# Kernel optimization log

Measured on AMD Instinct MI355X. Metric: run time of the kernel, lower is better.

The kernel has to match this reference:

```python
import jax, jax.numpy as jnp
import numpy as np

N_NODES = 100000
N_EDGES = 1600000
F_IN = 500
HIDDEN = 64
N_CLASS = 40


def gcn_conv(x, W, b, src, dst, n_nodes):
    """PyG GCNConv: add self-loops, symmetric deg^-1/2 normalization,
    linear transform then scatter-add aggregation at dst."""
    h = x @ W  # [N, out]
    loop = jnp.arange(n_nodes, dtype=src.dtype)
    s = jnp.concatenate([src, loop])  # sources incl. self-loops
    d = jnp.concatenate([dst, loop])
    deg = jax.ops.segment_sum(jnp.ones_like(d, dtype=h.dtype), d, num_segments=n_nodes)
    dinv = jnp.where(deg > 0, jax.lax.rsqrt(deg), 0.0)
    norm = dinv[s] * dinv[d]  # [E+N]
    msg = h[s] * norm[:, None]  # gather + scale, [E+N, out]
    out = jax.ops.segment_sum(msg, d, num_segments=n_nodes)
    return out + b


def setup_inputs() -> dict:
    key = jax.random.key(0)
    k1, k2, k3, k4 = jax.random.split(key, 4)
    x = jax.random.normal(k1, (N_NODES, F_IN), dtype=jnp.float32)
    edge_index = jax.random.randint(k2, (2, N_EDGES), 0, N_NODES, dtype=jnp.int64)
    # Glorot-style init for GCNConv weights
    W1 = jax.random.normal(k3, (F_IN, HIDDEN), dtype=jnp.float32) / np.sqrt(F_IN)
    b1 = jnp.zeros((HIDDEN,), dtype=jnp.float32)
    W2 = jax.random.normal(k4, (HIDDEN, N_CLASS), dtype=jnp.float32) / np.sqrt(HIDDEN)
    b2 = jnp.zeros((N_CLASS,), dtype=jnp.float32)
    return {"x": x, "W1": W1, "b1": b1, "W2": W2, "b2": b2, "edge_index": edge_index}


def reference(x, W1, b1, W2, b2, edge_index):
    src, dst = edge_index[0], edge_index[1]
    n = x.shape[0]
    h = jax.nn.relu(gcn_conv(x, W1, b1, src, dst, n))
    # dropout is identity in eval mode (F.dropout with training=False)
    out = gcn_conv(h, W2, b2, src, dst, n)
    return jax.nn.log_softmax(out, axis=1)
```

## Files before the change

kernel.cpp:

```cpp
#include <hip/hip_runtime.h>
#include <math.h>

#define N_NODES 100000
#define N_EDGES 1600000
#define F_IN    500
#define HIDDEN  64
#define N_CLASS 40
#define KPAD    512

#define NB   2048
#define NPB  49
#define EPB  16384
#define CAP  1536

typedef __attribute__((ext_vector_type(4))) float f32x4;
typedef __attribute__((ext_vector_type(8))) __bf16 bf16x8;

__device__ __forceinline__ unsigned short f2bf(float f) {
    unsigned int u = __float_as_uint(f);
    u = (u + 0x7FFF + ((u >> 16) & 1)) >> 16;
    return (unsigned short)u;
}

__global__ void k_zero_int(int* p, int n) {
    int i = blockIdx.x * blockDim.x + threadIdx.x;
    if (i < n) p[i] = 0;
}

__global__ void k_prep_w1t(const float* __restrict__ w1, unsigned short* __restrict__ w1t) {
    int idx = blockIdx.x * blockDim.x + threadIdx.x;
    if (idx >= HIDDEN * KPAD) return;
    int n = idx >> 9, k = idx & (KPAD - 1);
    float v = (k < F_IN) ? w1[k * HIDDEN + n] : 0.f;
    w1t[idx] = f2bf(v);
}

__launch_bounds__(1024)
__global__ void k_bhist(const int* __restrict__ dst, int* __restrict__ bcnt, int e) {
    __shared__ int h[NB];
    for (int i = threadIdx.x; i < NB; i += 1024) h[i] = 0;
    __syncthreads();
    int base = blockIdx.x * EPB;
#pragma unroll
    for (int j = 0; j < 16; ++j) {
        int i = base + j * 1024 + threadIdx.x;
        if (i < e) atomicAdd(&h[dst[i] / NPB], 1);
    }
    __syncthreads();
    for (int i = threadIdx.x; i < NB; i += 1024)
        if (h[i]) atomicAdd(&bcnt[i], h[i]);
}

__launch_bounds__(1024)
__global__ void k_bscan(const int* __restrict__ bcnt, int* __restrict__ bptr,
                        int* __restrict__ bcur) {
    __shared__ int s[1024];
    int t = threadIdx.x;
    int a = bcnt[2 * t], b = bcnt[2 * t + 1];
    int v = a + b;
    s[t] = v;
    __syncthreads();
    for (int off = 1; off < 1024; off <<= 1) {
        int u = (t >= off) ? s[t - off] : 0;
        __syncthreads();
        s[t] += u;
        __syncthreads();
    }
    int excl = s[t] - v;
    bptr[2 * t] = excl;     bptr[2 * t + 1] = excl + a;
    bcur[2 * t] = excl;     bcur[2 * t + 1] = excl + a;
    if (t == 1023) bptr[NB] = s[1023];
}

__launch_bounds__(1024)
__global__ void k_bfill(const int* __restrict__ src, const int* __restrict__ dst,
                        int* __restrict__ bcur, int2* __restrict__ ebuf, int e) {
    __shared__ int hist[NB];
    __shared__ int base_[NB];
    for (int i = threadIdx.x; i < NB; i += 1024) hist[i] = 0;
    __syncthreads();
    int b0 = blockIdx.x * EPB;
    int s_[16], d_[16];
#pragma unroll
    for (int j = 0; j < 16; ++j) {
        int i = b0 + j * 1024 + threadIdx.x;
        if (i < e) {
            s_[j] = src[i];
            d_[j] = dst[i];
            atomicAdd(&hist[d_[j] / NPB], 1);
        } else d_[j] = -1;
    }
    __syncthreads();
    for (int i = threadIdx.x; i < NB; i += 1024) {
        int hc = hist[i];
        base_[i] = hc ? atomicAdd(&bcur[i], hc) : 0;
        hist[i] = 0;
    }
    __syncthreads();
#pragma unroll
    for (int j = 0; j < 16; ++j) {
        if (d_[j] >= 0) {
            int bu = d_[j] / NPB;
            int r = atomicAdd(&hist[bu], 1);
            ebuf[base_[bu] + r] = make_int2(s_[j], d_[j]);
        }
    }
}

__launch_bounds__(256)
__global__ void k_bucket_csr(const int2* __restrict__ ebuf, const int* __restrict__ bptr,
                             int* __restrict__ rp, int* __restrict__ col,
                             float* __restrict__ dinv, int n) {
    int b  = blockIdx.x;
    int lo = b * NPB;
    if (lo >= n) return;
    int hi  = min(lo + NPB, n);
    int eb0 = bptr[b], ec = bptr[b + 1] - eb0;

    __shared__ int2 pairs[CAP];
    __shared__ int  hist[NPB];
    __shared__ int  excl[NPB + 1];
    for (int j = threadIdx.x; j < NPB; j += 256) hist[j] = 0;
    __syncthreads();
    for (int i = threadIdx.x; i < ec; i += 256) {
        int2 p = ebuf[eb0 + i];
        if (i < CAP) pairs[i] = p;
        atomicAdd(&hist[p.y - lo], 1);
    }
    __syncthreads();
    if (threadIdx.x == 0) {
        int acc = 0;
        for (int j = 0; j < NPB; ++j) { excl[j] = acc; acc += hist[j]; }
        excl[NPB] = acc;
    }
    __syncthreads();
    for (int j = threadIdx.x; j < hi - lo; j += 256) {
        rp[lo + j]   = eb0 + excl[j];
        dinv[lo + j] = rsqrtf((float)(hist[j] + 1));
    }
    if (hi == n && threadIdx.x == 0) rp[n] = eb0 + ec;
    __syncthreads();
    for (int j = threadIdx.x; j < NPB; j += 256) hist[j] = 0;
    __syncthreads();
    for (int i = threadIdx.x; i < ec; i += 256) {
        int2 p  = (i < CAP) ? pairs[i] : ebuf[eb0 + i];
        int  li = p.y - lo;
        int  r  = atomicAdd(&hist[li], 1);
        col[eb0 + excl[li] + r] = p.x;
    }
}

__launch_bounds__(256)
__global__ void k_gemm1(const float* __restrict__ x, const unsigned short* __restrict__ w1t,
                        float* __restrict__ h, int n) {
    __shared__ unsigned short xs[4][32][40];
    const int tid  = threadIdx.x;
    const int wave = tid >> 6;
    const int lane = tid & 63;
    const int quad = lane >> 4;
    const int l16  = lane & 15;
    const int rowb = blockIdx.x * 128 + wave * 32;

    const int srow = lane >> 3;
    const int skof = (lane & 7) * 4;

    f32x4 acc[2][4];
#pragma unroll
    for (int rt = 0; rt < 2; ++rt)
#pragma unroll
        for (int ct = 0; ct < 4; ++ct) acc[rt][ct] = (f32x4)0.f;

    for (int ks = 0; ks < 16; ++ks) {
        const int k0 = ks * 32;

        float4 tmp[4];
        if (ks < 15) {
#pragma unroll
            for (int u = 0; u < 4; ++u) {
                int grow = rowb + u * 8 + srow;
                tmp[u] = (grow < n) ? *(const float4*)&x[(size_t)grow * F_IN + k0 + skof]
                                    : make_float4(0.f, 0.f, 0.f, 0.f);
            }
        } else {
#pragma unroll
            for (int u = 0; u < 4; ++u) {
                int grow = rowb + u * 8 + srow;
                const float* p = &x[(size_t)grow * F_IN];
                float v0 = (grow < n && k0 + skof + 0 < F_IN) ? p[k0 + skof + 0] : 0.f;
                float v1 = (grow < n && k0 + skof + 1 < F_IN) ? p[k0 + skof + 1] : 0.f;
                float v2 = (grow < n && k0 + skof + 2 < F_IN) ? p[k0 + skof + 2] : 0.f;
                float v3 = (grow < n && k0 + skof + 3 < F_IN) ? p[k0 + skof + 3] : 0.f;
                tmp[u] = make_float4(v0, v1, v2, v3);
            }
        }
        bf16x8 bfrag[4];
#pragma unroll
        for (int ct = 0; ct < 4; ++ct)
            bfrag[ct] = *(const bf16x8*)&w1t[(ct * 16 + l16) * KPAD + k0 + quad * 8];

#pragma unroll
        for (int u = 0; u < 4; ++u) {
            unsigned int lo = (unsigned int)f2bf(tmp[u].x) | ((unsigned int)f2bf(tmp[u].y) << 16);
            unsigned int hi = (unsigned int)f2bf(tmp[u].z) | ((unsigned int)f2bf(tmp[u].w) << 16);
            *(uint2*)&xs[wave][u * 8 + srow][skof] = make_uint2(lo, hi);
        }
        __syncthreads();

        union { bf16x8 v; unsigned int u[4]; } af[2];
#pragma unroll
        for (int rt = 0; rt < 2; ++rt) {
            uint2 a = *(const uint2*)&xs[wave][rt * 16 + l16][quad * 8];
            uint2 b = *(const uint2*)&xs[wave][rt * 16 + l16][quad * 8 + 4];
            af[rt].u[0] = a.x; af[rt].u[1] = a.y; af[rt].u[2] = b.x; af[rt].u[3] = b.y;
        }
#pragma unroll
        for (int rt = 0; rt < 2; ++rt)
#pragma unroll
            for (int ct = 0; ct < 4; ++ct)
                acc[rt][ct] = __builtin_amdgcn_mfma_f32_16x16x32_bf16(
                    af[rt].v, bfrag[ct], acc[rt][ct], 0, 0, 0);
        __syncthreads();
    }

#pragma unroll
    for (int rt = 0; rt < 2; ++rt) {
#pragma unroll
        for (int reg = 0; reg < 4; ++reg) {
            int grow = rowb + rt * 16 + quad * 4 + reg;
            if (grow < n) {
#pragma unroll
                for (int ct = 0; ct < 4; ++ct)
                    h[(size_t)grow * HIDDEN + ct * 16 + l16] = acc[rt][ct][reg];
            }
        }
    }
}

template <int F, bool RELU, bool LSM>
__global__ void k_agg(const float* __restrict__ h, const int* __restrict__ rp,
                      const int* __restrict__ col, const float* __restrict__ dinv,
                      const float* __restrict__ bias, float* __restrict__ out, int n) {
    int wid  = (blockIdx.x * blockDim.x + threadIdx.x) >> 6;
    int lane = threadIdx.x & 63;
    if (wid >= n) return;
    int beg = rp[wid], end = rp[wid + 1];
    float acc = 0.f;
    int e = beg;
    for (; e + 4 <= end; e += 4) {
        int s0 = col[e], s1 = col[e + 1], s2 = col[e + 2], s3 = col[e + 3];
        float w0 = dinv[s0], w1 = dinv[s1], w2 = dinv[s2], w3 = dinv[s3];
        float h0 = (lane < F) ? h[(size_t)s0 * F + lane] : 0.f;
        float h1 = (lane < F) ? h[(size_t)s1 * F + lane] : 0.f;
        float h2 = (lane < F) ? h[(size_t)s2 * F + lane] : 0.f;
        float h3 = (lane < F) ? h[(size_t)s3 * F + lane] : 0.f;
        acc += w0 * h0 + w1 * h1 + w2 * h2 + w3 * h3;
    }
    for (; e < end; ++e) {
        int s0 = col[e];
        float w0 = dinv[s0];
        float h0 = (lane < F) ? h[(size_t)s0 * F + lane] : 0.f;
        acc += w0 * h0;
    }
    float di    = dinv[wid];
    float selfv = (lane < F) ? h[(size_t)wid * F + lane] : 0.f;
    float r = di * acc + di * di * selfv + ((lane < F) ? bias[lane] : 0.f);
    if (RELU) r = fmaxf(r, 0.f);
    if (LSM) {
        float v = (lane < F) ? r : -INFINITY;
        float m = v;
        for (int off = 32; off; off >>= 1) m = fmaxf(m, __shfl_xor(m, off));
        float ex = (lane < F) ? __expf(v - m) : 0.f;
        float s = ex;
        for (int off = 32; off; off >>= 1) s += __shfl_xor(s, off);
        if (lane < F) out[(size_t)wid * F + lane] = v - m - __logf(s);
    } else {
        if (lane < F) out[(size_t)wid * F + lane] = r;
    }
}

__launch_bounds__(256)
__global__ void k_gemm2(const float* __restrict__ a, const float* __restrict__ w,
                        float* __restrict__ out, int n) {
    __shared__ float ws[HIDDEN * N_CLASS];
    for (int idx = threadIdx.x; idx < HIDDEN * N_CLASS; idx += 256) ws[idx] = w[idx];
    __syncthreads();
    int idx = blockIdx.x * 256 + threadIdx.x;
    if (idx >= n * N_CLASS) return;
    int i = idx / N_CLASS, j = idx - i * N_CLASS;
    float s = 0.f;
#pragma unroll
    for (int k = 0; k < HIDDEN; k += 4) {
        float4 xv = *(const float4*)&a[(size_t)i * HIDDEN + k];
        s = fmaf(xv.x, ws[k * N_CLASS + j], s);
        s = fmaf(xv.y, ws[(k + 1) * N_CLASS + j], s);
        s = fmaf(xv.z, ws[(k + 2) * N_CLASS + j], s);
        s = fmaf(xv.w, ws[(k + 3) * N_CLASS + j], s);
    }
    out[idx] = s;
}

extern "C" void kernel_launch(void* const* d_in, const int* in_sizes, int n_in,
                              void* d_out, int out_size, void* d_ws, size_t ws_size,
                              hipStream_t stream) {
    const float* x   = (const float*)d_in[0];
    const float* W1  = (const float*)d_in[1];
    const float* b1  = (const float*)d_in[2];
    const float* W2  = (const float*)d_in[3];
    const float* b2  = (const float*)d_in[4];
    const int*   ei  = (const int*)d_in[5];
    const int*   src = ei;
    const int*   dst = ei + N_EDGES;
    float*       out = (float*)d_out;

    char*  ws  = (char*)d_ws;
    size_t off = 0;
    auto alloc = [&](size_t bytes) -> void* {
        void* p = ws + off;
        off += (bytes + 255) & ~(size_t)255;
        return p;
    };
    int*            bcnt = (int*)alloc((size_t)NB * 4);
    int*            bptr = (int*)alloc((size_t)(NB + 1) * 4);
    int*            bcur = (int*)alloc((size_t)NB * 4);
    int*            rp   = (int*)alloc((size_t)(N_NODES + 1) * 4);
    int*            col  = (int*)alloc((size_t)N_EDGES * 4);
    float*          dinv = (float*)alloc((size_t)N_NODES * 4);
    unsigned short* w1t  = (unsigned short*)alloc((size_t)HIDDEN * KPAD * 2);
    float*          h1   = (float*)alloc((size_t)N_NODES * HIDDEN * 4);
    float*          h1a  = (float*)alloc((size_t)N_NODES * HIDDEN * 4);
    int2*           ebuf = (int2*)h1a;
    float*          h2   = h1;

    const int NBH = (N_EDGES + EPB - 1) / EPB;

    k_zero_int<<<(NB + 255) / 256, 256, 0, stream>>>(bcnt, NB);
    k_prep_w1t<<<(HIDDEN * KPAD + 255) / 256, 256, 0, stream>>>(W1, w1t);
    k_bhist<<<NBH, 1024, 0, stream>>>(dst, bcnt, N_EDGES);
    k_bscan<<<1, 1024, 0, stream>>>(bcnt, bptr, bcur);
    k_bfill<<<NBH, 1024, 0, stream>>>(src, dst, bcur, ebuf, N_EDGES);
    k_bucket_csr<<<NB, 256, 0, stream>>>(ebuf, bptr, rp, col, dinv, N_NODES);

    k_gemm1<<<(N_NODES + 127) / 128, 256, 0, stream>>>(x, w1t, h1, N_NODES);
    k_agg<HIDDEN, true, false><<<(N_NODES + 3) / 4, 256, 0, stream>>>(h1, rp, col, dinv, b1, h1a, N_NODES);

    k_gemm2<<<(N_NODES * N_CLASS + 255) / 256, 256, 0, stream>>>(h1a, W2, h2, N_NODES);
    k_agg<N_CLASS, false, true><<<(N_NODES + 3) / 4, 256, 0, stream>>>(h2, rp, col, dinv, b2, out, N_NODES);
}
```

Baseline: 565.8 us.

## Store pre-scaled bf16 features and aggregate with paired-lane half-wave gathers

The GEMM epilogues now multiply each row by its source dinv and store the features as bf16, so each gathered message needs no per-edge dinv lookup and half the bytes. The aggregation kernel packs two features per 32-bit lane and splits edges between the two half-waves, then combines them with a shuffle. This targets gather bandwidth and dinv loads in the memory-bound aggregation. In exchange, intermediate features lose precision through bf16 rounding.

New measurement: 538.5 us. -4.8%, faster.

```diff
diff --git a/kernel.cpp b/kernel.cpp
--- a/kernel.cpp
+++ b/kernel.cpp
@@ -20,6 +20,12 @@
     unsigned int u = __float_as_uint(f);
     u = (u + 0x7FFF + ((u >> 16) & 1)) >> 16;
     return (unsigned short)u;
+}
+__device__ __forceinline__ float bfu_lo(unsigned int v) {
+    return __uint_as_float(v << 16);
+}
+__device__ __forceinline__ float bfu_hi(unsigned int v) {
+    return __uint_as_float(v & 0xFFFF0000u);
 }
 
 __global__ void k_zero_int(int* p, int n) {
@@ -152,7 +158,7 @@
 
 __launch_bounds__(256)
 __global__ void k_gemm1(const float* __restrict__ x, const unsigned short* __restrict__ w1t,
-                        float* __restrict__ h, int n) {
+                        const float* __restrict__ dinv, unsigned short* __restrict__ hs, int n) {
     __shared__ unsigned short xs[4][32][40];
     const int tid  = threadIdx.x;
     const int wave = tid >> 6;
@@ -228,59 +234,72 @@
         for (int reg = 0; reg < 4; ++reg) {
             int grow = rowb + rt * 16 + quad * 4 + reg;
             if (grow < n) {
+                float dv = dinv[grow];
 #pragma unroll
                 for (int ct = 0; ct < 4; ++ct)
-                    h[(size_t)grow * HIDDEN + ct * 16 + l16] = acc[rt][ct][reg];
+                    hs[(size_t)grow * HIDDEN + ct * 16 + l16] = f2bf(dv * acc[rt][ct][reg]);
             }
         }
     }
 }
 
 template <int F, bool RELU, bool LSM>
-__global__ void k_agg(const float* __restrict__ h, const int* __restrict__ rp,
+__global__ void k_agg(const unsigned int* __restrict__ hs, const int* __restrict__ rp,
                       const int* __restrict__ col, const float* __restrict__ dinv,
                       const float* __restrict__ bias, float* __restrict__ out, int n) {
+    constexpr int PW = F / 2;
     int wid  = (blockIdx.x * blockDim.x + threadIdx.x) >> 6;
-    int lane = threadIdx.x & 63;
+    wid = __builtin_amdgcn_readfirstlane(wid);
     if (wid >= n) return;
+    const int lane = threadIdx.x & 63;
+    const int half = lane >> 5;
+    const int p    = lane & 31;
+    const bool act = p < PW;
+
     int beg = rp[wid], end = rp[wid + 1];
-    float acc = 0.f;
-    int e = beg;
-    for (; e + 4 <= end; e += 4) {
-        int s0 = col[e], s1 = col[e + 1], s2 = col[e + 2], s3 = col[e + 3];
-        float w0 = dinv[s0], w1 = dinv[s1], w2 = dinv[s2], w3 = dinv[s3];
-        float h0 = (lane < F) ? h[(size_t)s0 * F + lane] : 0.f;
-        float h1 = (lane < F) ? h[(size_t)s1 * F + lane] : 0.f;
-        float h2 = (lane < F) ? h[(size_t)s2 * F + lane] : 0.f;
-        float h3 = (lane < F) ? h[(size_t)s3 * F + lane] : 0.f;
-        acc += w0 * h0 + w1 * h1 + w2 * h2 + w3 * h3;
-    }
-    for (; e < end; ++e) {
-        int s0 = col[e];
-        float w0 = dinv[s0];
-        float h0 = (lane < F) ? h[(size_t)s0 * F + lane] : 0.f;
-        acc += w0 * h0;
-    }
-    float di    = dinv[wid];
-    float selfv = (lane < F) ? h[(size_t)wid * F + lane] : 0.f;
-    float r = di * acc + di * di * selfv + ((lane < F) ? bias[lane] : 0.f);
-    if (RELU) r = fmaxf(r, 0.f);
+    float alo = 0.f, ahi = 0.f;
+    int e = beg + half;
+    for (; e + 6 < end; e += 8) {
+        int c0 = col[e], c1 = col[e + 2], c2 = col[e + 4], c3 = col[e + 6];
+        unsigned v0 = act ? hs[(unsigned)c0 * PW + p] : 0u;
+        unsigned v1 = act ? hs[(unsigned)c1 * PW + p] : 0u;
+        unsigned v2 = act ? hs[(unsigned)c2 * PW + p] : 0u;
+        unsigned v3 = act ? hs[(unsigned)c3 * PW + p] : 0u;
+        alo += bfu_lo(v0) + bfu_lo(v1) + bfu_lo(v2) + bfu_lo(v3);
+        ahi += bfu_hi(v0) + bfu_hi(v1) + bfu_hi(v2) + bfu_hi(v3);
+    }
+    for (; e < end; e += 2) {
+        int c0 = col[e];
+        unsigned v0 = act ? hs[(unsigned)c0 * PW + p] : 0u;
+        alo += bfu_lo(v0);
+        ahi += bfu_hi(v0);
+    }
+    alo += __shfl_xor(alo, 32);
+    ahi += __shfl_xor(ahi, 32);
+
+    float di = dinv[wid];
+    unsigned sv = act ? hs[(unsigned)wid * PW + p] : 0u;
+    float2 bv = act ? *(const float2*)&bias[2 * p] : make_float2(0.f, 0.f);
+    float rlo = di * (alo + bfu_lo(sv)) + bv.x;
+    float rhi = di * (ahi + bfu_hi(sv)) + bv.y;
+    if (RELU) { rlo = fmaxf(rlo, 0.f); rhi = fmaxf(rhi, 0.f); }
     if (LSM) {
-        float v = (lane < F) ? r : -INFINITY;
-        float m = v;
-        for (int off = 32; off; off >>= 1) m = fmaxf(m, __shfl_xor(m, off));
-        float ex = (lane < F) ? __expf(v - m) : 0.f;
-        float s = ex;
-        for (int off = 32; off; off >>= 1) s += __shfl_xor(s, off);
-        if (lane < F) out[(size_t)wid * F + lane] = v - m - __logf(s);
-    } else {
-        if (lane < F) out[(size_t)wid * F + lane] = r;
-    }
+        float m = act ? fmaxf(rlo, rhi) : -INFINITY;
+#pragma unroll
+        for (int off = 16; off; off >>= 1) m = fmaxf(m, __shfl_xor(m, off));
+        float ex = act ? (__expf(rlo - m) + __expf(rhi - m)) : 0.f;
+#pragma unroll
+        for (int off = 16; off; off >>= 1) ex += __shfl_xor(ex, off);
+        float lse = m + __logf(ex);
+        rlo -= lse; rhi -= lse;
+    }
+    if (half == 0 && act)
+        *(float2*)&out[(size_t)wid * F + 2 * p] = make_float2(rlo, rhi);
 }
 
 __launch_bounds__(256)
 __global__ void k_gemm2(const float* __restrict__ a, const float* __restrict__ w,
-                        float* __restrict__ out, int n) {
+                        const float* __restrict__ dinv, unsigned short* __restrict__ out, int n) {
     __shared__ float ws[HIDDEN * N_CLASS];
     for (int idx = threadIdx.x; idx < HIDDEN * N_CLASS; idx += 256) ws[idx] = w[idx];
     __syncthreads();
@@ -296,7 +315,7 @@
         s = fmaf(xv.z, ws[(k + 2) * N_CLASS + j], s);
         s = fmaf(xv.w, ws[(k + 3) * N_CLASS + j], s);
     }
-    out[idx] = s;
+    out[idx] = f2bf(dinv[i] * s);
 }
 
 extern "C" void kernel_launch(void* const* d_in, const int* in_sizes, int n_in,
@@ -326,10 +345,10 @@
     int*            col  = (int*)alloc((size_t)N_EDGES * 4);
     float*          dinv = (float*)alloc((size_t)N_NODES * 4);
     unsigned short* w1t  = (unsigned short*)alloc((size_t)HIDDEN * KPAD * 2);
-    float*          h1   = (float*)alloc((size_t)N_NODES * HIDDEN * 4);
+    unsigned short* h1s  = (unsigned short*)alloc((size_t)N_NODES * HIDDEN * 2);
     float*          h1a  = (float*)alloc((size_t)N_NODES * HIDDEN * 4);
     int2*           ebuf = (int2*)h1a;
-    float*          h2   = h1;
+    unsigned short* h2s  = h1s;
 
     const int NBH = (N_EDGES + EPB - 1) / EPB;
 
@@ -340,9 +359,11 @@
     k_bfill<<<NBH, 1024, 0, stream>>>(src, dst, bcur, ebuf, N_EDGES);
     k_bucket_csr<<<NB, 256, 0, stream>>>(ebuf, bptr, rp, col, dinv, N_NODES);
 
-    k_gemm1<<<(N_NODES + 127) / 128, 256, 0, stream>>>(x, w1t, h1, N_NODES);
-    k_agg<HIDDEN, true, false><<<(N_NODES + 3) / 4, 256, 0, stream>>>(h1, rp, col, dinv, b1, h1a, N_NODES);
-
-    k_gemm2<<<(N_NODES * N_CLASS + 255) / 256, 256, 0, stream>>>(h1a, W2, h2, N_NODES);
-    k_agg<N_CLASS, false, true><<<(N_NODES + 3) / 4, 256, 0, stream>>>(h2, rp, col, dinv, b2, out, N_NODES);
-}
+    k_gemm1<<<(N_NODES + 127) / 128, 256, 0, stream>>>(x, w1t, dinv, h1s, N_NODES);
+    k_agg<HIDDEN, true, false><<<(N_NODES + 3) / 4, 256, 0, stream>>>(
+        (const unsigned int*)h1s, rp, col, dinv, b1, h1a, N_NODES);
+
+    k_gemm2<<<(N_NODES * N_CLASS + 255) / 256, 256, 0, stream>>>(h1a, W2, dinv, h2s, N_NODES);
+    k_agg<N_CLASS, false, true><<<(N_NODES + 3) / 4, 256, 0, stream>>>(
+        (const unsigned int*)h2s, rp, col, dinv, b2, out, N_NODES);
+}
```
